# Optimization experiments

Measured on AMD Instinct MI355X. Metric: run time of the kernel, lower is better.

## Reference

```python
import jax, jax.numpy as jnp
import numpy as np

LN_EPS = 1e-5

def silu(x):
    return x * jax.nn.sigmoid(x)

def setup_inputs() -> dict:
    key = jax.random.key(0)
    ks = jax.random.split(key, 24)
    B, D = 131072, 256
    def w(k, shape, fan_in):
        return jax.random.uniform(k, shape, jnp.float32, -1.0, 1.0) / np.sqrt(fan_in)
    inp = {
        'x': jax.random.normal(ks[0], (B, D), jnp.float32),
        # stem: Linear(D,128) -> LN(128) -> SiLU -> Linear(128,64) -> SiLU
        'stem_w1': w(ks[1], (D, 128), D), 'stem_b1': w(ks[2], (128,), D),
        'ln_g': jnp.ones((128,), jnp.float32), 'ln_b': jnp.zeros((128,), jnp.float32),
        'stem_w2': w(ks[3], (128, 64), 128), 'stem_b2': w(ks[4], (64,), 128),
        # 4 experts: Linear(64,128)->SiLU->Linear(128,64)->SiLU, stacked on axis 0
        'ew1': w(ks[5], (4, 64, 128), 64), 'eb1': w(ks[6], (4, 128), 64),
        'ew2': w(ks[7], (4, 128, 64), 128), 'eb2': w(ks[8], (4, 64), 128),
        # gate: Linear(64,32)->SiLU->Linear(32,4)
        'gw1': w(ks[9], (64, 32), 64), 'gb1': w(ks[10], (32,), 64),
        'gw2': w(ks[11], (32, 4), 32), 'gb2': w(ks[12], (4,), 32),
        # shared: Linear(64,64)->SiLU
        'sw': w(ks[13], (64, 64), 64), 'sb': w(ks[14], (64,), 64),
        # 3 heads (strain, tensile, yield) stacked: Linear(64,32)->SiLU->Linear(32,1)
        'hw1': w(ks[15], (3, 64, 32), 64), 'hb1': w(ks[16], (3, 32), 64),
        'hw2': w(ks[17], (3, 32, 1), 32), 'hb2': w(ks[18], (3, 1), 32),
    }
    return inp

def reference(x, stem_w1, stem_b1, ln_g, ln_b, stem_w2, stem_b2,
              ew1, eb1, ew2, eb2, gw1, gb1, gw2, gb2, sw, sb,
              hw1, hb1, hw2, hb2):
    # stem (dropout = identity, eval mode)
    h = x @ stem_w1 + stem_b1                      # [B,128]
    mu = jnp.mean(h, -1, keepdims=True)
    var = jnp.mean(jnp.square(h - mu), -1, keepdims=True)
    h = (h - mu) * jax.lax.rsqrt(var + LN_EPS) * ln_g + ln_b
    h = silu(h)
    h = silu(h @ stem_w2 + stem_b2)                # [B,64]
    # gate
    g = silu(h @ gw1 + gb1)
    gate_w = jax.nn.softmax(g @ gw2 + gb2, axis=-1)  # [B,4]
    # experts: [B,64] x [4,64,128] -> [B,4,128]
    e = silu(jnp.einsum('bd,edh->beh', h, ew1) + eb1)
    e = silu(jnp.einsum('beh,ehd->bed', e, ew2) + eb2)  # [B,4,64]
    moe_h = jnp.einsum('bed,be->bd', e, gate_w)    # [B,64]
    # shared trunk (dropout = identity)
    feat = silu(moe_h @ sw + sb)                   # [B,64]
    # 3 heads
    hh = silu(jnp.einsum('bd,kdh->bkh', feat, hw1) + hb1)  # [B,3,32]
    out = (jnp.einsum('bkh,kho->bko', hh, hw2) + hb2)[..., 0]  # [B,3]
    return out
```

## Files before the change

kernel.cpp:

```cpp
#include <hip/hip_runtime.h>

typedef _Float16 f16;
typedef f16   f16x4 __attribute__((ext_vector_type(4)));
typedef f16   f16x8 __attribute__((ext_vector_type(8)));
typedef float f32x4 __attribute__((ext_vector_type(4)));

#define MFMA16(a, b, c) __builtin_amdgcn_mfma_f32_16x16x32_f16((a), (b), (c), 0, 0, 0)

#define IMG_W1   0
#define IMG_W2   32768
#define IMG_GW1  40960
#define IMG_EW1  43008
#define IMG_EW2  75776
#define IMG_SW   108544
#define IMG_HW1  112640

__device__ __forceinline__ float silu_f(float v) {
    return v * __builtin_amdgcn_rcpf(1.0f + __expf(-v));
}

__device__ void conv_blk(const float* __restrict__ src, f16* __restrict__ dst,
                         int srcN, int k0, int n0, int KB, int NB, int tid, int nth) {
    for (int i = tid; i < KB * NB; i += nth) {
        const int kk = i / NB, nn = i - kk * NB;
        dst[nn * KB + (kk ^ ((nn & 7) << 3))] = (f16)src[(long)(k0 + kk) * srcN + n0 + nn];
    }
}

__global__ void prep_weights(const float* __restrict__ w1, const float* __restrict__ w2,
                             const float* __restrict__ gw1, const float* __restrict__ ew1,
                             const float* __restrict__ ew2, const float* __restrict__ sw,
                             const float* __restrict__ hw1, f16* __restrict__ ws) {
    const int tid = blockIdx.x * 256 + threadIdx.x;
    const int nth = gridDim.x * 256;
    for (int kh = 0; kh < 2; ++kh)
        for (int nh = 0; nh < 2; ++nh)
            conv_blk(w1, ws + IMG_W1 + (kh * 2 + nh) * 8192, 128, kh * 128, nh * 64, 128, 64, tid, nth);
    conv_blk(w2,  ws + IMG_W2,  64, 0, 0, 128, 64, tid, nth);
    conv_blk(gw1, ws + IMG_GW1, 32, 0, 0,  64, 32, tid, nth);
    for (int e = 0; e < 4; ++e)
        for (int h = 0; h < 2; ++h) {
            conv_blk(ew1 + e * 8192, ws + IMG_EW1 + (e * 2 + h) * 4096, 128, 0, h * 64, 64, 64, tid, nth);
            conv_blk(ew2 + e * 8192, ws + IMG_EW2 + (e * 2 + h) * 4096,  64, h * 64, 0, 64, 64, tid, nth);
        }
    conv_blk(sw, ws + IMG_SW, 64, 0, 0, 64, 64, tid, nth);
    for (int h = 0; h < 3; ++h)
        conv_blk(hw1 + h * 2048, ws + IMG_HW1 + h * 2048, 32, 0, 0, 64, 32, tid, nth);
}

#define GLL16(g, l) __builtin_amdgcn_global_load_lds(                        \
    (const __attribute__((address_space(1))) void*)(g),                     \
    (__attribute__((address_space(3))) void*)(l), 16, 0, 0)

template<int S_F16>
__device__ __forceinline__ void stage_img(const f16* __restrict__ g, f16* l,
                                          int wv, int lane) {
    constexpr int QB = (S_F16 * 2) / 4;
    constexpr int CALLS = QB / 1024;
    const char* gs = (const char*)g + wv * QB + lane * 16;
    char* ls = (char*)l + wv * QB;
    #pragma unroll
    for (int i = 0; i < CALLS; ++i)
        GLL16(gs + i * 1024, ls + i * 1024);
}

__device__ __forceinline__ int swz_key(int mode, int r) {
    if (mode == 0) return (r & 7) << 3;
    if (mode == 1) return (r & 15) << 3;
    return ((((r >> 2) & 3) << 1) | (r & 1)) << 3;
}

template<int MODE>
__device__ __forceinline__ f16x8 ld_frag(const f16* base, int stride, int row_base, int k0) {
    const int lane = threadIdx.x & 63;
    const int r = row_base + (lane & 15);
    const int k = k0 + ((lane >> 4) << 3);
    return *(const f16x8*)(base + r * stride + (k ^ swz_key(MODE, r)));
}

template<int MODE>
__device__ __forceinline__ void st_frag(f16* base, int stride, int row_base, int col_base, f32x4 v) {
    const int lane = threadIdx.x & 63;
    const int c = col_base + (lane & 15);
    #pragma unroll
    for (int g = 0; g < 4; ++g) {
        const int r = row_base + ((lane >> 4) << 2) + g;
        base[r * stride + (c ^ swz_key(MODE, r))] = (f16)v[g];
    }
}

__device__ __forceinline__ void stage_x(const float* __restrict__ xsrc, f16* XACT, int half) {
    const int t = threadIdx.x;
    #pragma unroll 8
    for (int i = 0; i < 16; ++i) {
        const int idx4 = t + i * 256;
        const int r  = idx4 >> 5;
        const int kc = (idx4 & 31) << 2;
        const float4 v = *(const float4*)(xsrc + (long)r * 256 + half * 128 + kc);
        f16x4 o; o[0] = (f16)v.x; o[1] = (f16)v.y; o[2] = (f16)v.z; o[3] = (f16)v.w;
        *(f16x4*)(XACT + r * 128 + (kc ^ ((r & 15) << 3))) = o;
    }
}

__device__ __forceinline__ f32x4 reduce16(f32x4 v) {
    #pragma unroll
    for (int m = 1; m <= 8; m <<= 1) {
        f32x4 o;
        #pragma unroll
        for (int i = 0; i < 4; ++i) o[i] = __shfl_xor(v[i], m, 64);
        v += o;
    }
    return v;
}

__global__ __launch_bounds__(256, 3)
void fused_net_mfma(const float* __restrict__ x,   const f16* __restrict__ wsp,
                    const float* __restrict__ b1,  const float* __restrict__ lng,
                    const float* __restrict__ lnb, const float* __restrict__ b2,
                    const float* __restrict__ eb1, const float* __restrict__ eb2,
                    const float* __restrict__ gb1, const float* __restrict__ gw2,
                    const float* __restrict__ gb2, const float* __restrict__ sb,
                    const float* __restrict__ hb1, const float* __restrict__ hw2,
                    const float* __restrict__ hb2, float* __restrict__ out)
{
    __shared__ __align__(16) f16 lds[26624];
    f16* XACT = lds;
    f16* ACT1 = lds;
    f16* ACT2 = lds + 8192;
    f16* W    = lds + 16384;
    f16* G    = lds + 24576;

    const int lane = threadIdx.x & 63;
    const int wv   = threadIdx.x >> 6;
    const int c    = lane & 15;
    const long blockRow = (long)blockIdx.x * 128;
    const int waveRow = wv * 32;
    const float* xblk = x + blockRow * 256;

    f32x4 acc[2][8];
    #pragma unroll
    for (int n = 0; n < 8; ++n) {
        const float bv = b1[n * 16 + c];
        f32x4 t = {bv, bv, bv, bv};
        acc[0][n] = t; acc[1][n] = t;
    }
    #pragma unroll
    for (int kh = 0; kh < 2; ++kh) {
        if (kh) __syncthreads();
        stage_x(xblk, XACT, kh);
        stage_img<8192>(wsp + IMG_W1 + kh * 16384, W, wv, lane);
        __syncthreads();
        f16x8 af[2][4];
        #pragma unroll
        for (int m = 0; m < 2; ++m)
            #pragma unroll
            for (int ks = 0; ks < 4; ++ks)
                af[m][ks] = ld_frag<1>(XACT, 128, waveRow + m * 16, ks * 32);
        #pragma unroll
        for (int ks = 0; ks < 4; ++ks)
            #pragma unroll
            for (int n = 0; n < 4; ++n) {
                const f16x8 b = ld_frag<0>(W, 128, n * 16, ks * 32);
                acc[0][n] = MFMA16(af[0][ks], b, acc[0][n]);
                acc[1][n] = MFMA16(af[1][ks], b, acc[1][n]);
            }
        __syncthreads();
        stage_img<8192>(wsp + IMG_W1 + kh * 16384 + 8192, W, wv, lane);
        __syncthreads();
        #pragma unroll
        for (int ks = 0; ks < 4; ++ks)
            #pragma unroll
            for (int n = 0; n < 4; ++n) {
                const f16x8 b = ld_frag<0>(W, 128, n * 16, ks * 32);
                acc[0][4 + n] = MFMA16(af[0][ks], b, acc[0][4 + n]);
                acc[1][4 + n] = MFMA16(af[1][ks], b, acc[1][4 + n]);
            }
    }

    f32x4 mu[2], rs[2];
    #pragma unroll
    for (int m = 0; m < 2; ++m) {
        f32x4 s = {0, 0, 0, 0}, q = {0, 0, 0, 0};
        #pragma unroll
        for (int n = 0; n < 8; ++n) { s += acc[m][n]; q += acc[m][n] * acc[m][n]; }
        s = reduce16(s); q = reduce16(q);
        mu[m] = s * 0.0078125f;
        #pragma unroll
        for (int g = 0; g < 4; ++g) {
            const float var = q[g] * 0.0078125f - mu[m][g] * mu[m][g];
            rs[m][g] = rsqrtf(var + 1e-5f);
        }
    }
    __syncthreads();
    stage_img<8192>(wsp + IMG_W2,  W, wv, lane);
    stage_img<2048>(wsp + IMG_GW1, G, wv, lane);
    __syncthreads();

    f32x4 a2[2][4];
    #pragma unroll
    for (int n = 0; n < 4; ++n) {
        const float bv = b2[n * 16 + c];
        f32x4 t = {bv, bv, bv, bv};
        a2[0][n] = t; a2[1][n] = t;
    }
    #pragma unroll
    for (int half = 0; half < 2; ++half) {
        #pragma unroll
        for (int m = 0; m < 2; ++m)
            #pragma unroll
            for (int n = 0; n < 4; ++n) {
                const int j = half * 64 + n * 16 + c;
                const float gg = lng[j], bb = lnb[j];
                f32x4 v;
                #pragma unroll
                for (int g = 0; g < 4; ++g)
                    v[g] = silu_f((acc[m][half * 4 + n][g] - mu[m][g]) * rs[m][g] * gg + bb);
                st_frag<2>(ACT1, 64, waveRow + m * 16, n * 16, v);
            }
        #pragma unroll
        for (int ks = 0; ks < 2; ++ks) {
            const f16x8 a0 = ld_frag<2>(ACT1, 64, waveRow,      ks * 32);
            const f16x8 a1 = ld_frag<2>(ACT1, 64, waveRow + 16, ks * 32);
            #pragma unroll
            for (int n = 0; n < 4; ++n) {
                const f16x8 b = ld_frag<0>(W, 128, n * 16, half * 64 + ks * 32);
                a2[0][n] = MFMA16(a0, b, a2[0][n]);
                a2[1][n] = MFMA16(a1, b, a2[1][n]);
            }
        }
    }
    #pragma unroll
    for (int m = 0; m < 2; ++m)
        #pragma unroll
        for (int n = 0; n < 4; ++n) {
            f32x4 v;
            #pragma unroll
            for (int g = 0; g < 4; ++g) v[g] = silu_f(a2[m][n][g]);
            st_frag<2>(ACT2, 64, waveRow + m * 16, n * 16, v);
        }

    f32x4 gwt[2][4];
    {
        f32x4 ag[2][2];
        #pragma unroll
        for (int n = 0; n < 2; ++n) {
            const float bv = gb1[n * 16 + c];
            f32x4 t = {bv, bv, bv, bv};
            ag[0][n] = t; ag[1][n] = t;
        }
        #pragma unroll
        for (int ks = 0; ks < 2; ++ks) {
            const f16x8 a0 = ld_frag<2>(ACT2, 64, waveRow,      ks * 32);
            const f16x8 a1 = ld_frag<2>(ACT2, 64, waveRow + 16, ks * 32);
            #pragma unroll
            for (int n = 0; n < 2; ++n) {
                const f16x8 b = ld_frag<0>(G, 64, n * 16, ks * 32);
                ag[0][n] = MFMA16(a0, b, ag[0][n]);
                ag[1][n] = MFMA16(a1, b, ag[1][n]);
            }
        }
        const f32x4 gb2v = *(const f32x4*)gb2;
        #pragma unroll
        for (int m = 0; m < 2; ++m) {
            f32x4 pg[4] = {{0,0,0,0},{0,0,0,0},{0,0,0,0},{0,0,0,0}};
            #pragma unroll
            for (int n = 0; n < 2; ++n) {
                const int j = n * 16 + c;
                const f32x4 w4 = *(const f32x4*)(gw2 + j * 4);
                #pragma unroll
                for (int g = 0; g < 4; ++g)
                    pg[g] += silu_f(ag[m][n][g]) * w4;
            }
            #pragma unroll
            for (int g = 0; g < 4; ++g) {
                f32x4 l = reduce16(pg[g]) + gb2v;
                const float mx = fmaxf(fmaxf(l[0], l[1]), fmaxf(l[2], l[3]));
                f32x4 ee;
                #pragma unroll
                for (int o = 0; o < 4; ++o) ee[o] = __expf(l[o] - mx);
                const float inv = __builtin_amdgcn_rcpf(ee[0] + ee[1] + ee[2] + ee[3]);
                gwt[m][g] = ee * inv;
            }
        }
    }

    f32x4 moe[2][4] = {{{0,0,0,0},{0,0,0,0},{0,0,0,0},{0,0,0,0}},
                       {{0,0,0,0},{0,0,0,0},{0,0,0,0},{0,0,0,0}}};
    #pragma unroll
    for (int e = 0; e < 4; ++e) {
        f32x4 a2acc[2][4];
        #pragma unroll
        for (int n = 0; n < 4; ++n) {
            const float bv = eb2[e * 64 + n * 16 + c];
            f32x4 t = {bv, bv, bv, bv};
            a2acc[0][n] = t; a2acc[1][n] = t;
        }
        #pragma unroll
        for (int mh = 0; mh < 2; ++mh) {
            __syncthreads();
            stage_img<4096>(wsp + IMG_EW1 + (e * 2 + mh) * 4096, W,        wv, lane);
            stage_img<4096>(wsp + IMG_EW2 + (e * 2 + mh) * 4096, W + 4096, wv, lane);
            __syncthreads();
            f32x4 a1acc[2][4];
            #pragma unroll
            for (int n = 0; n < 4; ++n) {
                const float bv = eb1[e * 128 + mh * 64 + n * 16 + c];
                f32x4 t = {bv, bv, bv, bv};
                a1acc[0][n] = t; a1acc[1][n] = t;
            }
            #pragma unroll
            for (int ks = 0; ks < 2; ++ks) {
                const f16x8 a0 = ld_frag<2>(ACT2, 64, waveRow,      ks * 32);
                const f16x8 a1 = ld_frag<2>(ACT2, 64, waveRow + 16, ks * 32);
                #pragma unroll
                for (int n = 0; n < 4; ++n) {
                    const f16x8 b = ld_frag<0>(W, 64, n * 16, ks * 32);
                    a1acc[0][n] = MFMA16(a0, b, a1acc[0][n]);
                    a1acc[1][n] = MFMA16(a1, b, a1acc[1][n]);
                }
            }
            #pragma unroll
            for (int m = 0; m < 2; ++m)
                #pragma unroll
                for (int n = 0; n < 4; ++n) {
                    f32x4 v;
                    #pragma unroll
                    for (int g = 0; g < 4; ++g) v[g] = silu_f(a1acc[m][n][g]);
                    st_frag<2>(ACT1, 64, waveRow + m * 16, n * 16, v);
                }
            #pragma unroll
            for (int ks = 0; ks < 2; ++ks) {
                const f16x8 a0 = ld_frag<2>(ACT1, 64, waveRow,      ks * 32);
                const f16x8 a1 = ld_frag<2>(ACT1, 64, waveRow + 16, ks * 32);
                #pragma unroll
                for (int n = 0; n < 4; ++n) {
                    const f16x8 b = ld_frag<0>(W + 4096, 64, n * 16, ks * 32);
                    a2acc[0][n] = MFMA16(a0, b, a2acc[0][n]);
                    a2acc[1][n] = MFMA16(a1, b, a2acc[1][n]);
                }
            }
        }
        #pragma unroll
        for (int m = 0; m < 2; ++m)
            #pragma unroll
            for (int n = 0; n < 4; ++n)
                #pragma unroll
                for (int g = 0; g < 4; ++g)
                    moe[m][n][g] += silu_f(a2acc[m][n][g]) * gwt[m][g][e];
    }

    #pragma unroll
    for (int m = 0; m < 2; ++m)
        #pragma unroll
        for (int n = 0; n < 4; ++n)
            st_frag<2>(ACT2, 64, waveRow + m * 16, n * 16, moe[m][n]);
    __syncthreads();
    stage_img<4096>(wsp + IMG_SW,         W,        wv, lane);
    stage_img<2048>(wsp + IMG_HW1,        W + 4096, wv, lane);
    stage_img<2048>(wsp + IMG_HW1 + 2048, W + 6144, wv, lane);
    stage_img<2048>(wsp + IMG_HW1 + 4096, G,        wv, lane);
    __syncthreads();

    {
        f32x4 as[2][4];
        #pragma unroll
        for (int n = 0; n < 4; ++n) {
            const float bv = sb[n * 16 + c];
            f32x4 t = {bv, bv, bv, bv};
            as[0][n] = t; as[1][n] = t;
        }
        #pragma unroll
        for (int ks = 0; ks < 2; ++ks) {
            const f16x8 a0 = ld_frag<2>(ACT2, 64, waveRow,      ks * 32);
            const f16x8 a1 = ld_frag<2>(ACT2, 64, waveRow + 16, ks * 32);
            #pragma unroll
            for (int n = 0; n < 4; ++n) {
                const f16x8 b = ld_frag<0>(W, 64, n * 16, ks * 32);
                as[0][n] = MFMA16(a0, b, as[0][n]);
                as[1][n] = MFMA16(a1, b, as[1][n]);
            }
        }
        #pragma unroll
        for (int m = 0; m < 2; ++m)
            #pragma unroll
            for (int n = 0; n < 4; ++n) {
                f32x4 v;
                #pragma unroll
                for (int g = 0; g < 4; ++g) v[g] = silu_f(as[m][n][g]);
                st_frag<2>(ACT1, 64, waveRow + m * 16, n * 16, v);
            }
    }

    {
        f32x4 ah[2][6];
        #pragma unroll
        for (int n = 0; n < 6; ++n) {
            const float bv = hb1[(n >> 1) * 32 + (n & 1) * 16 + c];
            f32x4 t = {bv, bv, bv, bv};
            ah[0][n] = t; ah[1][n] = t;
        }
        #pragma unroll
        for (int ks = 0; ks < 2; ++ks) {
            const f16x8 a0 = ld_frag<2>(ACT1, 64, waveRow,      ks * 32);
            const f16x8 a1 = ld_frag<2>(ACT1, 64, waveRow + 16, ks * 32);
            #pragma unroll
            for (int n = 0; n < 6; ++n) {
                const int head = n >> 1;
                const f16* hw = (head == 0) ? (W + 4096) : (head == 1) ? (W + 6144) : G;
                const f16x8 b = ld_frag<0>(hw, 64, (n & 1) * 16, ks * 32);
                ah[0][n] = MFMA16(a0, b, ah[0][n]);
                ah[1][n] = MFMA16(a1, b, ah[1][n]);
            }
        }
        const float hb2_0 = hb2[0], hb2_1 = hb2[1], hb2_2 = hb2[2];
        #pragma unroll
        for (int m = 0; m < 2; ++m) {
            f32x4 ph[3] = {{0,0,0,0},{0,0,0,0},{0,0,0,0}};
            #pragma unroll
            for (int n = 0; n < 6; ++n) {
                const int head = n >> 1;
                const int j = (n & 1) * 16 + c;
                const float w2v = hw2[head * 32 + j];
                #pragma unroll
                for (int g = 0; g < 4; ++g)
                    ph[head][g] += silu_f(ah[m][n][g]) * w2v;
            }
            #pragma unroll
            for (int h = 0; h < 3; ++h) ph[h] = reduce16(ph[h]);
            #pragma unroll
            for (int g = 0; g < 4; ++g) {
                const long row = blockRow + waveRow + m * 16 + ((lane >> 4) << 2) + g;
                if (c < 3) {
                    const float r0 = ph[0][g] + hb2_0;
                    const float r1 = ph[1][g] + hb2_1;
                    const float r2 = ph[2][g] + hb2_2;
                    out[row * 3 + c] = (c == 0) ? r0 : ((c == 1) ? r1 : r2);
                }
            }
        }
    }
}

extern "C" void kernel_launch(void* const* d_in, const int* in_sizes, int n_in,
                              void* d_out, int out_size, void* d_ws, size_t ws_size,
                              hipStream_t stream) {
    const float* x    = (const float*)d_in[0];
    const float* w1   = (const float*)d_in[1];
    const float* b1   = (const float*)d_in[2];
    const float* lng  = (const float*)d_in[3];
    const float* lnb  = (const float*)d_in[4];
    const float* w2   = (const float*)d_in[5];
    const float* b2   = (const float*)d_in[6];
    const float* ew1  = (const float*)d_in[7];
    const float* eb1  = (const float*)d_in[8];
    const float* ew2  = (const float*)d_in[9];
    const float* eb2  = (const float*)d_in[10];
    const float* gw1  = (const float*)d_in[11];
    const float* gb1  = (const float*)d_in[12];
    const float* gw2  = (const float*)d_in[13];
    const float* gb2  = (const float*)d_in[14];
    const float* sw   = (const float*)d_in[15];
    const float* sb   = (const float*)d_in[16];
    const float* hw1  = (const float*)d_in[17];
    const float* hb1  = (const float*)d_in[18];
    const float* hw2  = (const float*)d_in[19];
    const float* hb2  = (const float*)d_in[20];
    float* out = (float*)d_out;
    f16* ws = (f16*)d_ws;

    hipLaunchKernelGGL(prep_weights, dim3(64), dim3(256), 0, stream,
                       w1, w2, gw1, ew1, ew2, sw, hw1, ws);

    const int B = in_sizes[0] / 256;
    const int grid = B / 128;
    hipLaunchKernelGGL(fused_net_mfma, dim3(grid), dim3(256), 0, stream,
                       x, ws, b1, lng, lnb, b2, eb1, eb2, gb1, gw2, gb2,
                       sb, hb1, hw2, hb2, out);
}
```

Measured before the change: 109.1 us.

## Split fused network into stem, expert and head kernels with weights resident in LDS

The single fused kernel is split into three kernels: stem plus gate, experts, and shared trunk plus heads. Each uses 768-thread blocks of 12 waves in which every wave owns a 32-row tile. Each kernel stages its whole weight set into LDS once per block instead of restaging weight slices between block-wide barriers, and x is read straight from global into MFMA fragments instead of through LDS. This removes most __syncthreads and weight-restaging traffic, but adds global round-trips for the intermediate activations and gate weights plus two extra kernel launches.

```diff
diff --git a/kernel.cpp b/kernel.cpp
--- a/kernel.cpp
+++ b/kernel.cpp
@@ -1,7 +1,6 @@
 #include <hip/hip_runtime.h>
 
 typedef _Float16 f16;
-typedef f16   f16x4 __attribute__((ext_vector_type(4)));
 typedef f16   f16x8 __attribute__((ext_vector_type(8)));
 typedef float f32x4 __attribute__((ext_vector_type(4)));
 
@@ -10,10 +9,14 @@
 #define IMG_W1   0
 #define IMG_W2   32768
 #define IMG_GW1  40960
-#define IMG_EW1  43008
-#define IMG_EW2  75776
+#define IMG_E    43008
 #define IMG_SW   108544
 #define IMG_HW1  112640
+#define HB_F16   118784
+#define MOE_F16  8507392
+#define GWT_F16  16896000
+
+#define NW 12
 
 __device__ __forceinline__ float silu_f(float v) {
     return v * __builtin_amdgcn_rcpf(1.0f + __expf(-v));
@@ -40,8 +43,8 @@
     conv_blk(gw1, ws + IMG_GW1, 32, 0, 0,  64, 32, tid, nth);
     for (int e = 0; e < 4; ++e)
         for (int h = 0; h < 2; ++h) {
-            conv_blk(ew1 + e * 8192, ws + IMG_EW1 + (e * 2 + h) * 4096, 128, 0, h * 64, 64, 64, tid, nth);
-            conv_blk(ew2 + e * 8192, ws + IMG_EW2 + (e * 2 + h) * 4096,  64, h * 64, 0, 64, 64, tid, nth);
+            conv_blk(ew1 + e * 8192, ws + IMG_E + e * 16384 + h * 4096,        128, 0, h * 64, 64, 64, tid, nth);
+            conv_blk(ew2 + e * 8192, ws + IMG_E + e * 16384 + 8192 + h * 4096,  64, h * 64, 0, 64, 64, tid, nth);
         }
     conv_blk(sw, ws + IMG_SW, 64, 0, 0, 64, 64, tid, nth);
     for (int h = 0; h < 3; ++h)
@@ -52,21 +55,17 @@
     (const __attribute__((address_space(1))) void*)(g),                     \
     (__attribute__((address_space(3))) void*)(l), 16, 0, 0)
 
-template<int S_F16>
-__device__ __forceinline__ void stage_img(const f16* __restrict__ g, f16* l,
-                                          int wv, int lane) {
-    constexpr int QB = (S_F16 * 2) / 4;
-    constexpr int CALLS = QB / 1024;
-    const char* gs = (const char*)g + wv * QB + lane * 16;
-    char* ls = (char*)l + wv * QB;
-    #pragma unroll
-    for (int i = 0; i < CALLS; ++i)
-        GLL16(gs + i * 1024, ls + i * 1024);
+template<int BYTES>
+__device__ __forceinline__ void stage12(const f16* __restrict__ g, f16* l, int wv, int lane) {
+    constexpr int CALLS = BYTES / 1024;
+    #pragma unroll
+    for (int ch = 0; ch < CALLS; ++ch)
+        if (ch % NW == wv)
+            GLL16((const char*)g + ch * 1024 + lane * 16, (char*)l + ch * 1024);
 }
 
 __device__ __forceinline__ int swz_key(int mode, int r) {
     if (mode == 0) return (r & 7) << 3;
-    if (mode == 1) return (r & 15) << 3;
     return ((((r >> 2) & 3) << 1) | (r & 1)) << 3;
 }
 
@@ -89,17 +88,15 @@
     }
 }
 
-__device__ __forceinline__ void stage_x(const float* __restrict__ xsrc, f16* XACT, int half) {
-    const int t = threadIdx.x;
-    #pragma unroll 8
-    for (int i = 0; i < 16; ++i) {
-        const int idx4 = t + i * 256;
-        const int r  = idx4 >> 5;
-        const int kc = (idx4 & 31) << 2;
-        const float4 v = *(const float4*)(xsrc + (long)r * 256 + half * 128 + kc);
-        f16x4 o; o[0] = (f16)v.x; o[1] = (f16)v.y; o[2] = (f16)v.z; o[3] = (f16)v.w;
-        *(f16x4*)(XACT + r * 128 + (kc ^ ((r & 15) << 3))) = o;
-    }
+__device__ __forceinline__ f16x8 ld_x(const float* __restrict__ xrb, int ks) {
+    const int lane = threadIdx.x & 63;
+    const float* p = xrb + (long)(lane & 15) * 256 + ks * 32 + ((lane >> 4) << 3);
+    const float4 u = *(const float4*)p;
+    const float4 w = *(const float4*)(p + 4);
+    f16x8 a;
+    a[0] = (f16)u.x; a[1] = (f16)u.y; a[2] = (f16)u.z; a[3] = (f16)u.w;
+    a[4] = (f16)w.x; a[5] = (f16)w.y; a[6] = (f16)w.z; a[7] = (f16)w.w;
+    return a;
 }
 
 __device__ __forceinline__ f32x4 reduce16(f32x4 v) {
@@ -113,29 +110,29 @@
     return v;
 }
 
-__global__ __launch_bounds__(256, 3)
-void fused_net_mfma(const float* __restrict__ x,   const f16* __restrict__ wsp,
-                    const float* __restrict__ b1,  const float* __restrict__ lng,
-                    const float* __restrict__ lnb, const float* __restrict__ b2,
-                    const float* __restrict__ eb1, const float* __restrict__ eb2,
-                    const float* __restrict__ gb1, const float* __restrict__ gw2,
-                    const float* __restrict__ gb2, const float* __restrict__ sb,
-                    const float* __restrict__ hb1, const float* __restrict__ hw2,
-                    const float* __restrict__ hb2, float* __restrict__ out)
+__global__ __launch_bounds__(768, 3)
+void stem_kernel(const float* __restrict__ x,   const f16* __restrict__ wsp,
+                 const float* __restrict__ b1,  const float* __restrict__ lng,
+                 const float* __restrict__ lnb, const float* __restrict__ b2,
+                 const float* __restrict__ gb1, const float* __restrict__ gw2,
+                 const float* __restrict__ gb2,
+                 f16* __restrict__ hb_img, float* __restrict__ gwt_img, int NT)
 {
-    __shared__ __align__(16) f16 lds[26624];
-    f16* XACT = lds;
-    f16* ACT1 = lds;
-    f16* ACT2 = lds + 8192;
-    f16* W    = lds + 16384;
-    f16* G    = lds + 24576;
-
+    __shared__ __align__(16) f16 lds[43008 + NW * 2048];
+    f16* W1  = lds;
+    f16* W2  = lds + 32768;
+    f16* GW1 = lds + 40960;
     const int lane = threadIdx.x & 63;
     const int wv   = threadIdx.x >> 6;
     const int c    = lane & 15;
-    const long blockRow = (long)blockIdx.x * 128;
-    const int waveRow = wv * 32;
-    const float* xblk = x + blockRow * 256;
+    const int q    = lane >> 4;
+    f16* STR = lds + 43008 + wv * 2048;
+
+    stage12<86016>(wsp, lds, wv, lane);
+    __syncthreads();
+
+    const int tile = blockIdx.x * NW + wv;
+    if (tile >= NT) return;
 
     f32x4 acc[2][8];
     #pragma unroll
@@ -144,57 +141,32 @@
         f32x4 t = {bv, bv, bv, bv};
         acc[0][n] = t; acc[1][n] = t;
     }
-    #pragma unroll
-    for (int kh = 0; kh < 2; ++kh) {
-        if (kh) __syncthreads();
-        stage_x(xblk, XACT, kh);
-        stage_img<8192>(wsp + IMG_W1 + kh * 16384, W, wv, lane);
-        __syncthreads();
-        f16x8 af[2][4];
-        #pragma unroll
-        for (int m = 0; m < 2; ++m)
-            #pragma unroll
-            for (int ks = 0; ks < 4; ++ks)
-                af[m][ks] = ld_frag<1>(XACT, 128, waveRow + m * 16, ks * 32);
-        #pragma unroll
-        for (int ks = 0; ks < 4; ++ks)
-            #pragma unroll
-            for (int n = 0; n < 4; ++n) {
-                const f16x8 b = ld_frag<0>(W, 128, n * 16, ks * 32);
-                acc[0][n] = MFMA16(af[0][ks], b, acc[0][n]);
-                acc[1][n] = MFMA16(af[1][ks], b, acc[1][n]);
-            }
-        __syncthreads();
-        stage_img<8192>(wsp + IMG_W1 + kh * 16384 + 8192, W, wv, lane);
-        __syncthreads();
-        #pragma unroll
-        for (int ks = 0; ks < 4; ++ks)
-            #pragma unroll
-            for (int n = 0; n < 4; ++n) {
-                const f16x8 b = ld_frag<0>(W, 128, n * 16, ks * 32);
-                acc[0][4 + n] = MFMA16(af[0][ks], b, acc[0][4 + n]);
-                acc[1][4 + n] = MFMA16(af[1][ks], b, acc[1][4 + n]);
-            }
+    const float* xt = x + (long)tile * 32 * 256;
+    #pragma unroll
+    for (int ks = 0; ks < 8; ++ks) {
+        const f16x8 a0 = ld_x(xt,            ks);
+        const f16x8 a1 = ld_x(xt + 16 * 256, ks);
+        const int kh = ks >> 2, ksl = ks & 3;
+        #pragma unroll
+        for (int nf = 0; nf < 8; ++nf) {
+            const f16x8 b = ld_frag<0>(W1 + (kh * 2 + (nf >> 2)) * 8192, 128, (nf & 3) * 16, ksl * 32);
+            acc[0][nf] = MFMA16(a0, b, acc[0][nf]);
+            acc[1][nf] = MFMA16(a1, b, acc[1][nf]);
+        }
     }
 
     f32x4 mu[2], rs[2];
     #pragma unroll
     for (int m = 0; m < 2; ++m) {
-        f32x4 s = {0, 0, 0, 0}, q = {0, 0, 0, 0};
-        #pragma unroll
-        for (int n = 0; n < 8; ++n) { s += acc[m][n]; q += acc[m][n] * acc[m][n]; }
-        s = reduce16(s); q = reduce16(q);
+        f32x4 s = {0,0,0,0}, qq = {0,0,0,0};
+        #pragma unroll
+        for (int n = 0; n < 8; ++n) { s += acc[m][n]; qq += acc[m][n] * acc[m][n]; }
+        s = reduce16(s); qq = reduce16(qq);
         mu[m] = s * 0.0078125f;
         #pragma unroll
-        for (int g = 0; g < 4; ++g) {
-            const float var = q[g] * 0.0078125f - mu[m][g] * mu[m][g];
-            rs[m][g] = rsqrtf(var + 1e-5f);
-        }
-    }
-    __syncthreads();
-    stage_img<8192>(wsp + IMG_W2,  W, wv, lane);
-    stage_img<2048>(wsp + IMG_GW1, G, wv, lane);
-    __syncthreads();
+        for (int g = 0; g < 4; ++g)
+            rs[m][g] = rsqrtf(qq[g] * 0.0078125f - mu[m][g] * mu[m][g] + 1e-5f);
+    }
 
     f32x4 a2[2][4];
     #pragma unroll
@@ -215,15 +187,15 @@
                 #pragma unroll
                 for (int g = 0; g < 4; ++g)
                     v[g] = silu_f((acc[m][half * 4 + n][g] - mu[m][g]) * rs[m][g] * gg + bb);
-                st_frag<2>(ACT1, 64, waveRow + m * 16, n * 16, v);
+                st_frag<2>(STR, 64, m * 16, n * 16, v);
             }
         #pragma unroll
         for (int ks = 0; ks < 2; ++ks) {
-            const f16x8 a0 = ld_frag<2>(ACT1, 64, waveRow,      ks * 32);
-            const f16x8 a1 = ld_frag<2>(ACT1, 64, waveRow + 16, ks * 32);
+            const f16x8 a0 = ld_frag<2>(STR, 64, 0,  ks * 32);
+            const f16x8 a1 = ld_frag<2>(STR, 64, 16, ks * 32);
             #pragma unroll
             for (int n = 0; n < 4; ++n) {
-                const f16x8 b = ld_frag<0>(W, 128, n * 16, half * 64 + ks * 32);
+                const f16x8 b = ld_frag<0>(W2, 128, n * 16, half * 64 + ks * 32);
                 a2[0][n] = MFMA16(a0, b, a2[0][n]);
                 a2[1][n] = MFMA16(a1, b, a2[1][n]);
             }
@@ -236,206 +208,271 @@
             f32x4 v;
             #pragma unroll
             for (int g = 0; g < 4; ++g) v[g] = silu_f(a2[m][n][g]);
-            st_frag<2>(ACT2, 64, waveRow + m * 16, n * 16, v);
-        }
-
-    f32x4 gwt[2][4];
-    {
-        f32x4 ag[2][2];
+            st_frag<2>(STR, 64, m * 16, n * 16, v);
+        }
+    f16x8 hbA[2][2];
+    #pragma unroll
+    for (int m = 0; m < 2; ++m)
+        #pragma unroll
+        for (int ks = 0; ks < 2; ++ks) {
+            hbA[m][ks] = ld_frag<2>(STR, 64, m * 16, ks * 32);
+            *(f16x8*)(hb_img + (((long)tile * 2 + m) * 2 + ks) * 512 + lane * 8) = hbA[m][ks];
+        }
+
+    f32x4 ag[2][2];
+    #pragma unroll
+    for (int n = 0; n < 2; ++n) {
+        const float bv = gb1[n * 16 + c];
+        f32x4 t = {bv, bv, bv, bv};
+        ag[0][n] = t; ag[1][n] = t;
+    }
+    #pragma unroll
+    for (int ks = 0; ks < 2; ++ks)
         #pragma unroll
         for (int n = 0; n < 2; ++n) {
-            const float bv = gb1[n * 16 + c];
-            f32x4 t = {bv, bv, bv, bv};
-            ag[0][n] = t; ag[1][n] = t;
-        }
-        #pragma unroll
-        for (int ks = 0; ks < 2; ++ks) {
-            const f16x8 a0 = ld_frag<2>(ACT2, 64, waveRow,      ks * 32);
-            const f16x8 a1 = ld_frag<2>(ACT2, 64, waveRow + 16, ks * 32);
-            #pragma unroll
-            for (int n = 0; n < 2; ++n) {
-                const f16x8 b = ld_frag<0>(G, 64, n * 16, ks * 32);
-                ag[0][n] = MFMA16(a0, b, ag[0][n]);
-                ag[1][n] = MFMA16(a1, b, ag[1][n]);
-            }
-        }
-        const f32x4 gb2v = *(const f32x4*)gb2;
-        #pragma unroll
-        for (int m = 0; m < 2; ++m) {
-            f32x4 pg[4] = {{0,0,0,0},{0,0,0,0},{0,0,0,0},{0,0,0,0}};
-            #pragma unroll
-            for (int n = 0; n < 2; ++n) {
-                const int j = n * 16 + c;
-                const f32x4 w4 = *(const f32x4*)(gw2 + j * 4);
-                #pragma unroll
-                for (int g = 0; g < 4; ++g)
-                    pg[g] += silu_f(ag[m][n][g]) * w4;
-            }
-            #pragma unroll
-            for (int g = 0; g < 4; ++g) {
-                f32x4 l = reduce16(pg[g]) + gb2v;
-                const float mx = fmaxf(fmaxf(l[0], l[1]), fmaxf(l[2], l[3]));
-                f32x4 ee;
-                #pragma unroll
-                for (int o = 0; o < 4; ++o) ee[o] = __expf(l[o] - mx);
-                const float inv = __builtin_amdgcn_rcpf(ee[0] + ee[1] + ee[2] + ee[3]);
-                gwt[m][g] = ee * inv;
-            }
-        }
-    }
+            const f16x8 b = ld_frag<0>(GW1, 64, n * 16, ks * 32);
+            ag[0][n] = MFMA16(hbA[0][ks], b, ag[0][n]);
+            ag[1][n] = MFMA16(hbA[1][ks], b, ag[1][n]);
+        }
+    const f32x4 gb2v = *(const f32x4*)gb2;
+    #pragma unroll
+    for (int m = 0; m < 2; ++m) {
+        f32x4 pg[4] = {{0,0,0,0},{0,0,0,0},{0,0,0,0},{0,0,0,0}};
+        #pragma unroll
+        for (int n = 0; n < 2; ++n) {
+            const f32x4 w4 = *(const f32x4*)(gw2 + (n * 16 + c) * 4);
+            #pragma unroll
+            for (int g = 0; g < 4; ++g)
+                pg[g] += silu_f(ag[m][n][g]) * w4;
+        }
+        f32x4 gwt[4];
+        #pragma unroll
+        for (int g = 0; g < 4; ++g) {
+            f32x4 l = reduce16(pg[g]) + gb2v;
+            const float mx = fmaxf(fmaxf(l[0], l[1]), fmaxf(l[2], l[3]));
+            f32x4 ee;
+            #pragma unroll
+            for (int o = 0; o < 4; ++o) ee[o] = __expf(l[o] - mx);
+            gwt[g] = ee * __builtin_amdgcn_rcpf(ee[0] + ee[1] + ee[2] + ee[3]);
+        }
+        if (c < 4) {
+            float4 o;
+            o.x = (c == 0) ? gwt[0][0] : (c == 1) ? gwt[0][1] : (c == 2) ? gwt[0][2] : gwt[0][3];
+            o.y = (c == 0) ? gwt[1][0] : (c == 1) ? gwt[1][1] : (c == 2) ? gwt[1][2] : gwt[1][3];
+            o.z = (c == 0) ? gwt[2][0] : (c == 1) ? gwt[2][1] : (c == 2) ? gwt[2][2] : gwt[2][3];
+            o.w = (c == 0) ? gwt[3][0] : (c == 1) ? gwt[3][1] : (c == 2) ? gwt[3][2] : gwt[3][3];
+            *(float4*)(gwt_img + ((long)tile * 4 + c) * 32 + m * 16 + q * 4) = o;
+        }
+    }
+}
+
+__global__ __launch_bounds__(768, 3)
+void expert_kernel(const f16* __restrict__ wsp, const float* __restrict__ eb1,
+                   const float* __restrict__ eb2,
+                   const f16* __restrict__ hb_img, const float* __restrict__ gwt_img,
+                   f16* __restrict__ moe_img, int NT)
+{
+    __shared__ __align__(16) f16 lds[32768 + NW * 2048];
+    f16* EW = lds;
+    const int lane = threadIdx.x & 63;
+    const int wv   = threadIdx.x >> 6;
+    const int c    = lane & 15;
+    const int q    = lane >> 4;
+    f16* STR = lds + 32768 + wv * 2048;
+
+    const int tile = blockIdx.x * NW + wv;
+    const bool act = tile < NT;
+
+    f16x8 hbA[2][2];
+    if (act)
+        #pragma unroll
+        for (int m = 0; m < 2; ++m)
+            #pragma unroll
+            for (int ks = 0; ks < 2; ++ks)
+                hbA[m][ks] = *(const f16x8*)(hb_img + (((long)tile * 2 + m) * 2 + ks) * 512 + lane * 8);
 
     f32x4 moe[2][4] = {{{0,0,0,0},{0,0,0,0},{0,0,0,0},{0,0,0,0}},
                        {{0,0,0,0},{0,0,0,0},{0,0,0,0},{0,0,0,0}}};
-    #pragma unroll
-    for (int e = 0; e < 4; ++e) {
-        f32x4 a2acc[2][4];
-        #pragma unroll
-        for (int n = 0; n < 4; ++n) {
-            const float bv = eb2[e * 64 + n * 16 + c];
-            f32x4 t = {bv, bv, bv, bv};
-            a2acc[0][n] = t; a2acc[1][n] = t;
-        }
-        #pragma unroll
-        for (int mh = 0; mh < 2; ++mh) {
-            __syncthreads();
-            stage_img<4096>(wsp + IMG_EW1 + (e * 2 + mh) * 4096, W,        wv, lane);
-            stage_img<4096>(wsp + IMG_EW2 + (e * 2 + mh) * 4096, W + 4096, wv, lane);
-            __syncthreads();
-            f32x4 a1acc[2][4];
-            #pragma unroll
-            for (int n = 0; n < 4; ++n) {
-                const float bv = eb1[e * 128 + mh * 64 + n * 16 + c];
-                f32x4 t = {bv, bv, bv, bv};
-                a1acc[0][n] = t; a1acc[1][n] = t;
-            }
-            #pragma unroll
-            for (int ks = 0; ks < 2; ++ks) {
-                const f16x8 a0 = ld_frag<2>(ACT2, 64, waveRow,      ks * 32);
-                const f16x8 a1 = ld_frag<2>(ACT2, 64, waveRow + 16, ks * 32);
+
+    #pragma unroll
+    for (int p = 0; p < 2; ++p) {
+        if (p) __syncthreads();
+        stage12<65536>(wsp + IMG_E + p * 32768, EW, wv, lane);
+        __syncthreads();
+        if (act) {
+            #pragma unroll
+            for (int el = 0; el < 2; ++el) {
+                const int ee = p * 2 + el;
+                const f16* ebase = EW + el * 16384;
+                f32x4 a2acc[2][4];
                 #pragma unroll
                 for (int n = 0; n < 4; ++n) {
-                    const f16x8 b = ld_frag<0>(W, 64, n * 16, ks * 32);
-                    a1acc[0][n] = MFMA16(a0, b, a1acc[0][n]);
-                    a1acc[1][n] = MFMA16(a1, b, a1acc[1][n]);
+                    const float bv = eb2[ee * 64 + n * 16 + c];
+                    f32x4 t = {bv, bv, bv, bv};
+                    a2acc[0][n] = t; a2acc[1][n] = t;
+                }
+                #pragma unroll
+                for (int mh = 0; mh < 2; ++mh) {
+                    f32x4 a1acc[2][4];
+                    #pragma unroll
+                    for (int n = 0; n < 4; ++n) {
+                        const float bv = eb1[ee * 128 + mh * 64 + n * 16 + c];
+                        f32x4 t = {bv, bv, bv, bv};
+                        a1acc[0][n] = t; a1acc[1][n] = t;
+                    }
+                    #pragma unroll
+                    for (int ks = 0; ks < 2; ++ks)
+                        #pragma unroll
+                        for (int n = 0; n < 4; ++n) {
+                            const f16x8 b = ld_frag<0>(ebase + mh * 4096, 64, n * 16, ks * 32);
+                            a1acc[0][n] = MFMA16(hbA[0][ks], b, a1acc[0][n]);
+                            a1acc[1][n] = MFMA16(hbA[1][ks], b, a1acc[1][n]);
+                        }
+                    #pragma unroll
+                    for (int m = 0; m < 2; ++m)
+                        #pragma unroll
+                        for (int n = 0; n < 4; ++n) {
+                            f32x4 v;
+                            #pragma unroll
+                            for (int g = 0; g < 4; ++g) v[g] = silu_f(a1acc[m][n][g]);
+                            st_frag<2>(STR, 64, m * 16, n * 16, v);
+                        }
+                    #pragma unroll
+                    for (int ks = 0; ks < 2; ++ks) {
+                        const f16x8 a0 = ld_frag<2>(STR, 64, 0,  ks * 32);
+                        const f16x8 a1 = ld_frag<2>(STR, 64, 16, ks * 32);
+                        #pragma unroll
+                        for (int n = 0; n < 4; ++n) {
+                            const f16x8 b = ld_frag<0>(ebase + 8192 + mh * 4096, 64, n * 16, ks * 32);
+                            a2acc[0][n] = MFMA16(a0, b, a2acc[0][n]);
+                            a2acc[1][n] = MFMA16(a1, b, a2acc[1][n]);
+                        }
+                    }
+                }
+                const float* gb = gwt_img + ((long)tile * 4 + ee) * 32 + q * 4;
+                #pragma unroll
+                for (int m = 0; m < 2; ++m) {
+                    const float4 g4 = *(const float4*)(gb + m * 16);
+                    #pragma unroll
+                    for (int n = 0; n < 4; ++n) {
+                        moe[m][n][0] += silu_f(a2acc[m][n][0]) * g4.x;
+                        moe[m][n][1] += silu_f(a2acc[m][n][1]) * g4.y;
+                        moe[m][n][2] += silu_f(a2acc[m][n][2]) * g4.z;
+                        moe[m][n][3] += silu_f(a2acc[m][n][3]) * g4.w;
+                    }
                 }
             }
-            #pragma unroll
-            for (int m = 0; m < 2; ++m)
-                #pragma unroll
-                for (int n = 0; n < 4; ++n) {
-                    f32x4 v;
-                    #pragma unroll
-                    for (int g = 0; g < 4; ++g) v[g] = silu_f(a1acc[m][n][g]);
-                    st_frag<2>(ACT1, 64, waveRow + m * 16, n * 16, v);
-                }
-            #pragma unroll
-            for (int ks = 0; ks < 2; ++ks) {
-                const f16x8 a0 = ld_frag<2>(ACT1, 64, waveRow,      ks * 32);
-                const f16x8 a1 = ld_frag<2>(ACT1, 64, waveRow + 16, ks * 32);
-                #pragma unroll
-                for (int n = 0; n < 4; ++n) {
-                    const f16x8 b = ld_frag<0>(W + 4096, 64, n * 16, ks * 32);
-                    a2acc[0][n] = MFMA16(a0, b, a2acc[0][n]);
-                    a2acc[1][n] = MFMA16(a1, b, a2acc[1][n]);
-                }
-            }
-        }
-        #pragma unroll
-        for (int m = 0; m < 2; ++m)
-            #pragma unroll
-            for (int n = 0; n < 4; ++n)
-                #pragma unroll
-                for (int g = 0; g < 4; ++g)
-                    moe[m][n][g] += silu_f(a2acc[m][n][g]) * gwt[m][g][e];
-    }
-
+        }
+    }
+    if (!act) return;
     #pragma unroll
     for (int m = 0; m < 2; ++m)
         #pragma unroll
         for (int n = 0; n < 4; ++n)
-            st_frag<2>(ACT2, 64, waveRow + m * 16, n * 16, moe[m][n]);
+            st_frag<2>(STR, 64, m * 16, n * 16, moe[m][n]);
+    #pragma unroll
+    for (int m = 0; m < 2; ++m)
+        #pragma unroll
+        for (int ks = 0; ks < 2; ++ks)
+            *(f16x8*)(moe_img + (((long)tile * 2 + m) * 2 + ks) * 512 + lane * 8) =
+                ld_frag<2>(STR, 64, m * 16, ks * 32);
+}
+
+__global__ __launch_bounds__(768, 3)
+void head_kernel(const f16* __restrict__ wsp, const float* __restrict__ sb,
+                 const float* __restrict__ hb1, const float* __restrict__ hw2,
+                 const float* __restrict__ hb2, const f16* __restrict__ moe_img,
+                 float* __restrict__ out, int NT)
+{
+    __shared__ __align__(16) f16 lds[10240 + NW * 2048];
+    f16* SW  = lds;
+    f16* HW1 = lds + 4096;
+    const int lane = threadIdx.x & 63;
+    const int wv   = threadIdx.x >> 6;
+    const int c    = lane & 15;
+    f16* STR = lds + 10240 + wv * 2048;
+
+    stage12<20480>(wsp + IMG_SW, lds, wv, lane);
     __syncthreads();
-    stage_img<4096>(wsp + IMG_SW,         W,        wv, lane);
-    stage_img<2048>(wsp + IMG_HW1,        W + 4096, wv, lane);
-    stage_img<2048>(wsp + IMG_HW1 + 2048, W + 6144, wv, lane);
-    stage_img<2048>(wsp + IMG_HW1 + 4096, G,        wv, lane);
-    __syncthreads();
-
-    {
-        f32x4 as[2][4];
+
+    const int tile = blockIdx.x * NW + wv;
+    if (tile >= NT) return;
+
+    f16x8 moeA[2][2];
+    #pragma unroll
+    for (int m = 0; m < 2; ++m)
+        #pragma unroll
+        for (int ks = 0; ks < 2; ++ks)
+            moeA[m][ks] = *(const f16x8*)(moe_img + (((long)tile * 2 + m) * 2 + ks) * 512 + lane * 8);
+
+    f32x4 as[2][4];
+    #pragma unroll
+    for (int n = 0; n < 4; ++n) {
+        const float bv = sb[n * 16 + c];
+        f32x4 t = {bv, bv, bv, bv};
+        as[0][n] = t; as[1][n] = t;
+    }
+    #pragma unroll
+    for (int ks = 0; ks < 2; ++ks)
         #pragma unroll
         for (int n = 0; n < 4; ++n) {
-            const float bv = sb[n * 16 + c];
-            f32x4 t = {bv, bv, bv, bv};
-            as[0][n] = t; as[1][n] = t;
-        }
-        #pragma unroll
-        for (int ks = 0; ks < 2; ++ks) {
-            const f16x8 a0 = ld_frag<2>(ACT2, 64, waveRow,      ks * 32);
-            const f16x8 a1 = ld_frag<2>(ACT2, 64, waveRow + 16, ks * 32);
-            #pragma unroll
-            for (int n = 0; n < 4; ++n) {
-                const f16x8 b = ld_frag<0>(W, 64, n * 16, ks * 32);
-                as[0][n] = MFMA16(a0, b, as[0][n]);
-                as[1][n] = MFMA16(a1, b, as[1][n]);
-            }
-        }
-        #pragma unroll
-        for (int m = 0; m < 2; ++m)
-            #pragma unroll
-            for (int n = 0; n < 4; ++n) {
-                f32x4 v;
-                #pragma unroll
-                for (int g = 0; g < 4; ++g) v[g] = silu_f(as[m][n][g]);
-                st_frag<2>(ACT1, 64, waveRow + m * 16, n * 16, v);
-            }
-    }
-
-    {
-        f32x4 ah[2][6];
+            const f16x8 b = ld_frag<0>(SW, 64, n * 16, ks * 32);
+            as[0][n] = MFMA16(moeA[0][ks], b, as[0][n]);
+            as[1][n] = MFMA16(moeA[1][ks], b, as[1][n]);
+        }
+    #pragma unroll
+    for (int m = 0; m < 2; ++m)
+        #pragma unroll
+        for (int n = 0; n < 4; ++n) {
+            f32x4 v;
+            #pragma unroll
+            for (int g = 0; g < 4; ++g) v[g] = silu_f(as[m][n][g]);
+            st_frag<2>(STR, 64, m * 16, n * 16, v);
+        }
+    f16x8 featA[2][2];
+    #pragma unroll
+    for (int m = 0; m < 2; ++m)
+        #pragma unroll
+        for (int ks = 0; ks < 2; ++ks)
+            featA[m][ks] = ld_frag<2>(STR, 64, m * 16, ks * 32);
+
+    f32x4 ah[2][6];
+    #pragma unroll
+    for (int n = 0; n < 6; ++n) {
+        const float bv = hb1[(n >> 1) * 32 + (n & 1) * 16 + c];
+        f32x4 t = {bv, bv, bv, bv};
+        ah[0][n] = t; ah[1][n] = t;
+    }
+    #pragma unroll
+    for (int ks = 0; ks < 2; ++ks)
         #pragma unroll
         for (int n = 0; n < 6; ++n) {
-            const float bv = hb1[(n >> 1) * 32 + (n & 1) * 16 + c];
-            f32x4 t = {bv, bv, bv, bv};
-            ah[0][n] = t; ah[1][n] = t;
-        }
-        #pragma unroll
-        for (int ks = 0; ks < 2; ++ks) {
-            const f16x8 a0 = ld_frag<2>(ACT1, 64, waveRow,      ks * 32);
-            const f16x8 a1 = ld_frag<2>(ACT1, 64, waveRow + 16, ks * 32);
-            #pragma unroll
-            for (int n = 0; n < 6; ++n) {
-                const int head = n >> 1;
-                const f16* hw = (head == 0) ? (W + 4096) : (head == 1) ? (W + 6144) : G;
-                const f16x8 b = ld_frag<0>(hw, 64, (n & 1) * 16, ks * 32);
-                ah[0][n] = MFMA16(a0, b, ah[0][n]);
-                ah[1][n] = MFMA16(a1, b, ah[1][n]);
-            }
-        }
-        const float hb2_0 = hb2[0], hb2_1 = hb2[1], hb2_2 = hb2[2];
-        #pragma unroll
-        for (int m = 0; m < 2; ++m) {
-            f32x4 ph[3] = {{0,0,0,0},{0,0,0,0},{0,0,0,0}};
-            #pragma unroll
-            for (int n = 0; n < 6; ++n) {
-                const int head = n >> 1;
-                const int j = (n & 1) * 16 + c;
-                const float w2v = hw2[head * 32 + j];
-                #pragma unroll
-                for (int g = 0; g < 4; ++g)
-                    ph[head][g] += silu_f(ah[m][n][g]) * w2v;
-            }
-            #pragma unroll
-            for (int h = 0; h < 3; ++h) ph[h] = reduce16(ph[h]);
-            #pragma unroll
-            for (int g = 0; g < 4; ++g) {
-                const long row = blockRow + waveRow + m * 16 + ((lane >> 4) << 2) + g;
-                if (c < 3) {
-                    const float r0 = ph[0][g] + hb2_0;
-                    const float r1 = ph[1][g] + hb2_1;
-                    const float r2 = ph[2][g] + hb2_2;
-                    out[row * 3 + c] = (c == 0) ? r0 : ((c == 1) ? r1 : r2);
-                }
+            const f16x8 b = ld_frag<0>(HW1 + (n >> 1) * 2048, 64, (n & 1) * 16, ks * 32);
+            ah[0][n] = MFMA16(featA[0][ks], b, ah[0][n]);
+            ah[1][n] = MFMA16(featA[1][ks], b, ah[1][n]);
+        }
+    const float hb2_0 = hb2[0], hb2_1 = hb2[1], hb2_2 = hb2[2];
+    #pragma unroll
+    for (int m = 0; m < 2; ++m) {
+        f32x4 ph[3] = {{0,0,0,0},{0,0,0,0},{0,0,0,0}};
+        #pragma unroll
+        for (int n = 0; n < 6; ++n) {
+            const int head = n >> 1;
+            const float w2v = hw2[head * 32 + (n & 1) * 16 + c];
+            #pragma unroll
+            for (int g = 0; g < 4; ++g)
+                ph[head][g] += silu_f(ah[m][n][g]) * w2v;
+        }
+        #pragma unroll
+        for (int h = 0; h < 3; ++h) ph[h] = reduce16(ph[h]);
+        #pragma unroll
+        for (int g = 0; g < 4; ++g) {
+            const long row = (long)tile * 32 + m * 16 + ((lane >> 4) << 2) + g;
+            if (c < 3) {
+                const float r0 = ph[0][g] + hb2_0;
+                const float r1 = ph[1][g] + hb2_1;
+                const float r2 = ph[2][g] + hb2_2;
+                out[row * 3 + c] = (c == 0) ? r0 : ((c == 1) ? r1 : r2);
             }
         }
     }
@@ -466,14 +503,22 @@
     const float* hw2  = (const float*)d_in[19];
     const float* hb2  = (const float*)d_in[20];
     float* out = (float*)d_out;
-    f16* ws = (f16*)d_ws;
+
+    f16*   ws      = (f16*)d_ws;
+    f16*   hb_img  = ws + HB_F16;
+    f16*   moe_img = ws + MOE_F16;
+    float* gwt_img = (float*)(ws + GWT_F16);
+
+    const int B  = in_sizes[0] / 256;
+    const int NT = B / 32;
+    const int grid = (NT + NW - 1) / NW;
 
     hipLaunchKernelGGL(prep_weights, dim3(64), dim3(256), 0, stream,
                        w1, w2, gw1, ew1, ew2, sw, hw1, ws);
-
-    const int B = in_sizes[0] / 256;
-    const int grid = B / 128;
-    hipLaunchKernelGGL(fused_net_mfma, dim3(grid), dim3(256), 0, stream,
-                       x, ws, b1, lng, lnb, b2, eb1, eb2, gb1, gw2, gb2,
-                       sb, hb1, hw2, hb2, out);
-}
+    hipLaunchKernelGGL(stem_kernel, dim3(grid), dim3(NW * 64), 0, stream,
+                       x, ws, b1, lng, lnb, b2, gb1, gw2, gb2, hb_img, gwt_img, NT);
+    hipLaunchKernelGGL(expert_kernel, dim3(grid), dim3(NW * 64), 0, stream,
+                       ws, eb1, eb2, hb_img, gwt_img, moe_img, NT);
+    hipLaunchKernelGGL(head_kernel, dim3(grid), dim3(NW * 64), 0, stream,
+                       ws, sb, hb1, hw2, hb2, moe_img, out, NT);
+}
```

Measured after the change: 145.6 us. 1.33x slower.
